# Kernel tuning notes

Measured on AMD Instinct MI355X. Metric: run time of the kernel, lower is better.

## Reference

```python
import jax, jax.numpy as jnp
import numpy as np

HEAD_NUM = 16
SCALE = 1.0 / np.sqrt(HEAD_NUM)  # source divides by sqrt(head_num), not head_dim
MASK_VAL = -10000000.0


def setup_inputs() -> dict:
    key = jax.random.key(0)
    kq, kk, kv = jax.random.split(key, 3)
    shape = (2, 16, 2048, 64)  # [B, H, L, D]
    Q = jax.random.normal(kq, shape, dtype=jnp.float32)
    K = jax.random.normal(kk, shape, dtype=jnp.float32)
    V = jax.random.normal(kv, shape, dtype=jnp.float32)
    return {"Q": Q, "K": K, "V": V}


def reference(Q, K, V):
    L = Q.shape[-2]
    # [B, H, L, M] attention logits, scaled by 1/sqrt(head_num)
    logits = jnp.einsum('bhld,bhmd->bhlm', Q, K) * SCALE
    # causal mask: strictly-upper triangle gets -1e7 (additive, as in source)
    mask = jnp.triu(jnp.ones((L, L), dtype=logits.dtype), 1) * MASK_VAL
    logits = logits + mask[None, None, :, :]
    weights = jax.nn.softmax(logits, axis=-1)
    return jnp.einsum('bhlm,bhmd->bhld', weights, V)
```

## Files before the change

### kernel.cpp

```cpp
#include <hip/hip_runtime.h>
#include <hip/hip_bf16.h>

#define BM 128
#define BN 64
#define HD 64
#define LQ 2048
#define SD 72

typedef __attribute__((ext_vector_type(8))) short short8;
typedef __attribute__((ext_vector_type(16))) float f32x16;

#define QSCALE 0.360673760222241f

#define WS_HALF  ((size_t)32 * 2048 * 64)
#define WS_NEEDED (2 * WS_HALF * sizeof(unsigned short))

static __device__ __forceinline__ unsigned pk2(float a, float b) {
    union { __hip_bfloat162 h2; unsigned u; } c;
    c.h2 = __float22bfloat162_rn(make_float2(a, b));
    return c.u;
}

__global__ __launch_bounds__(256)
void prep(const float* __restrict__ Kg, const float* __restrict__ Vg,
          unsigned short* __restrict__ KF, unsigned short* __restrict__ VF) {
    __shared__ unsigned short sK2[64][72];
    __shared__ unsigned short sV2[64][72];
    const int t  = threadIdx.x;
    const int bx = blockIdx.x;
    const int bh = bx >> 5;
    const int c  = bx & 31;
    const size_t ibase = (size_t)bh * (LQ * HD) + (size_t)c * 64 * HD;
    const int r  = t >> 4;
    const int c4 = (t & 15) * 4;

#pragma unroll
    for (int p = 0; p < 4; ++p) {
        const int row = p * 16 + r;
        const float4 kv4 = *(const float4*)(Kg + ibase + (size_t)row * HD + c4);
        uint2 ku; ku.x = pk2(kv4.x, kv4.y); ku.y = pk2(kv4.z, kv4.w);
        *(uint2*)&sK2[row][c4] = ku;
        const float4 vv4 = *(const float4*)(Vg + ibase + (size_t)row * HD + c4);
        const unsigned u0 = pk2(vv4.x, vv4.y);
        const unsigned u1 = pk2(vv4.z, vv4.w);
        sV2[c4 + 0][row] = (unsigned short)(u0 & 0xffff);
        sV2[c4 + 1][row] = (unsigned short)(u0 >> 16);
        sV2[c4 + 2][row] = (unsigned short)(u1 & 0xffff);
        sV2[c4 + 3][row] = (unsigned short)(u1 >> 16);
    }
    __syncthreads();

    const int lane = t & 63;
    const int u    = t >> 6;
    const int l31  = lane & 31;
    const int hh   = lane >> 5;
#pragma unroll
    for (int e = 0; e < 2; ++e) {
        const int ch = 2 * c + e;
        const size_t ob = ((size_t)(bh * 64 + ch) * 4 + u) * 512 + lane * 8;
        *(uint4*)&KF[ob] = *(const uint4*)&sK2[e * 32 + l31][u * 16 + hh * 8];
        *(uint4*)&VF[ob] = *(const uint4*)&sV2[(u & 1) * 32 + l31][e * 32 + (u >> 1) * 16 + hh * 8];
    }
}

__global__ __launch_bounds__(512, 4)
void fa_main(const float* __restrict__ Qg,
             const unsigned short* __restrict__ KF,
             const unsigned short* __restrict__ VF,
             float* __restrict__ Og) {
    __shared__ float fx[4 * 64 * 32];
    __shared__ float fla[4 * 32];

    const int t    = threadIdx.x;
    const int w    = t >> 6;
    const int lane = t & 63;
    const int h    = lane >> 5;
    const int l31  = lane & 31;
    const int qg   = w & 3;
    const int kp   = w >> 2;

    const int bx  = blockIdx.x;
    const int idx = (bx >> 5) & 7;
    const int qt  = (bx & 256) ? idx : (15 - idx);
    const int bh  = bx & 31;
    const int q0  = qt * BM;

    const size_t base = (size_t)bh * (LQ * HD);
    const unsigned short* KFh = KF + (size_t)bh * 131072 + lane * 8;
    const unsigned short* VFh = VF + (size_t)bh * 131072 + lane * 8;

    const int j    = 4 * qt + qg;
    const int qrow = j * 32 + l31;

    short8 qreg[4];
    {
        const float* Qrow = Qg + base + (size_t)qrow * HD;
#pragma unroll
        for (int ks = 0; ks < 4; ++ks) {
            const float4 a = *(const float4*)(Qrow + ks * 16 + h * 8);
            const float4 b = *(const float4*)(Qrow + ks * 16 + h * 8 + 4);
            union { unsigned u[4]; short8 s8; } qu;
            qu.u[0] = pk2(a.x * QSCALE, a.y * QSCALE);
            qu.u[1] = pk2(a.z * QSCALE, a.w * QSCALE);
            qu.u[2] = pk2(b.x * QSCALE, b.y * QSCALE);
            qu.u[3] = pk2(b.z * QSCALE, b.w * QSCALE);
            qreg[ks] = qu.s8;
        }
    }

    f32x16 accO[2];
#pragma unroll
    for (int r = 0; r < 16; ++r) { accO[0][r] = 0.f; accO[1][r] = 0.f; }
    float lsum = 0.f;

    auto loadK = [&](short8* ak, int ch) {
        const unsigned short* kpt = KFh + (size_t)ch * 2048;
        ak[0] = *(const short8*)(kpt);
        ak[1] = *(const short8*)(kpt + 512);
        ak[2] = *(const short8*)(kpt + 1024);
        ak[3] = *(const short8*)(kpt + 1536);
    };

    auto computech = [&](const short8* ak, short8* akNext, int ch, bool pre) {
        short8 av[4];
        const unsigned short* vp = VFh + (size_t)ch * 2048;
        av[0] = *(const short8*)(vp);
        av[1] = *(const short8*)(vp + 512);
        av[2] = *(const short8*)(vp + 1024);
        av[3] = *(const short8*)(vp + 1536);
        if (pre) loadK(akNext, ch + 2);
        __builtin_amdgcn_sched_barrier(0);

        f32x16 accS;
#pragma unroll
        for (int r = 0; r < 16; ++r) accS[r] = 0.f;
        __builtin_amdgcn_s_setprio(1);
#pragma unroll
        for (int ks = 0; ks < 4; ++ks)
            accS = __builtin_amdgcn_mfma_f32_32x32x16_bf16(ak[ks], qreg[ks], accS, 0, 0, 0);
        __builtin_amdgcn_s_setprio(0);

        if (ch == j) {
            const int kvb = ch * 32 + 4 * h;
#pragma unroll
            for (int r = 0; r < 16; ++r) {
                const int kv = kvb + (r & 3) + 8 * (r >> 2);
                if (kv > qrow) accS[r] = -1e30f;
            }
        }

#pragma unroll
        for (int r = 0; r < 16; ++r) {
            const float p = __builtin_amdgcn_exp2f(accS[r]);
            accS[r] = p;
            lsum += p;
        }

        short8 pf[2];
#pragma unroll
        for (int s = 0; s < 2; ++s) {
            const int rb = s * 8;
            const unsigned a0 = pk2(accS[rb + 0], accS[rb + 1]);
            const unsigned b0 = pk2(accS[rb + 4], accS[rb + 5]);
            const unsigned a1 = pk2(accS[rb + 2], accS[rb + 3]);
            const unsigned b1 = pk2(accS[rb + 6], accS[rb + 7]);
            const auto r02 = __builtin_amdgcn_permlane32_swap(a0, b0, 0, 0);
            const auto r13 = __builtin_amdgcn_permlane32_swap(a1, b1, 0, 0);
            union { unsigned u[4]; short8 s8; } pu;
            pu.u[0] = r02[0]; pu.u[1] = r13[0]; pu.u[2] = r02[1]; pu.u[3] = r13[1];
            pf[s] = pu.s8;
        }

        __builtin_amdgcn_s_setprio(1);
#pragma unroll
        for (int s = 0; s < 2; ++s)
#pragma unroll
            for (int dg = 0; dg < 2; ++dg)
                accO[dg] = __builtin_amdgcn_mfma_f32_32x32x16_bf16(av[s * 2 + dg], pf[s], accO[dg], 0, 0, 0);
        __builtin_amdgcn_s_setprio(0);
    };

    short8 akA[4], akB[4];
    int ch = kp;
    if (ch <= j) {
        loadK(akA, ch);
        for (;;) {
            computech(akA, akB, ch, ch + 2 <= j);
            ch += 2;
            if (ch > j) break;
            computech(akB, akA, ch, ch + 2 <= j);
            ch += 2;
            if (ch > j) break;
        }
    }

    lsum += __shfl_xor(lsum, 32);
    if (kp == 1) {
#pragma unroll
        for (int dg = 0; dg < 2; ++dg) {
#pragma unroll
            for (int r = 0; r < 16; ++r) {
                const int d = dg * 32 + (r & 3) + 8 * (r >> 2) + 4 * h;
                fx[(qg * 64 + d) * 32 + l31] = accO[dg][r];
            }
        }
        if (h == 0) fla[qg * 32 + l31] = lsum;
    }
    __syncthreads();
    if (kp == 0) {
        const float inv = 1.0f / (lsum + fla[qg * 32 + l31]);
        float* Op = Og + base + (size_t)qrow * HD;
#pragma unroll
        for (int dg = 0; dg < 2; ++dg) {
#pragma unroll
            for (int rq = 0; rq < 4; ++rq) {
                const int d = dg * 32 + 8 * rq + 4 * h;
                const float* fr = &fx[(qg * 64 + d) * 32 + l31];
                float4 o;
                o.x = (accO[dg][rq * 4 + 0] + fr[0])  * inv;
                o.y = (accO[dg][rq * 4 + 1] + fr[32]) * inv;
                o.z = (accO[dg][rq * 4 + 2] + fr[64]) * inv;
                o.w = (accO[dg][rq * 4 + 3] + fr[96]) * inv;
                *(float4*)(Op + d) = o;
            }
        }
    }
}

__global__ __launch_bounds__(512, 4)
void fa_fwd(const float* __restrict__ Qg,
            const float* __restrict__ Kg,
            const float* __restrict__ Vg,
            float* __restrict__ Og) {
    __shared__ __align__(16) unsigned short lds[(2 * BN + 2 * HD) * SD];
    typedef unsigned short KT[BN][SD];
    typedef unsigned short VT[HD][SD];
    KT* sK  = (KT*)lds;
    VT* sVt = (VT*)(lds + 2 * BN * SD);

    const int t    = threadIdx.x;
    const int w    = t >> 6;
    const int lane = t & 63;
    const int h    = lane >> 5;
    const int l31  = lane & 31;
    const int qd   = lane >> 4;
    const int qg   = w & 3;
    const int kh   = w >> 2;

    const int bx  = blockIdx.x;
    const int idx = (bx >> 5) & 7;
    const int qt  = (bx & 256) ? idx : (15 - idx);
    const int bh  = bx & 31;
    const int q0  = qt * BM;

    const size_t base = (size_t)bh * (LQ * HD);
    const float* Qp = Qg + base + (size_t)q0 * HD;
    const float* Kp = Kg + base;
    const float* Vp = Vg + base;

    const int r0 = t >> 4;
    const int c4 = (t & 15) * 4;
    const int RA = w * 4;

    {
        unsigned short (*sQ)[SD] = (unsigned short (*)[SD])lds;
#pragma unroll
        for (int p = 0; p < 4; ++p) {
            const int r = p * 32 + r0;
            const float4 v = *(const float4*)(Qp + (size_t)r * HD + c4);
            uint2 u;
            u.x = pk2(v.x * QSCALE, v.y * QSCALE);
            u.y = pk2(v.z * QSCALE, v.w * QSCALE);
            *(uint2*)&sQ[r][c4] = u;
        }
    }
    __syncthreads();
    short8 qreg[4];
    {
        unsigned short (*sQ)[SD] = (unsigned short (*)[SD])lds;
#pragma unroll
        for (int ks = 0; ks < 4; ++ks)
            qreg[ks] = *(const short8*)&sQ[qg * 32 + l31][ks * 16 + h * 8];
    }
    __syncthreads();

    float4 kA, kB, vA, vB;
    auto issue = [&](int kv0) {
        kA = *(const float4*)(Kp + (size_t)(kv0 + r0) * HD + c4);
        kB = *(const float4*)(Kp + (size_t)(kv0 + 32 + r0) * HD + c4);
        vA = *(const float4*)(Vp + (size_t)(kv0 + RA + qd) * HD + c4);
        vB = *(const float4*)(Vp + (size_t)(kv0 + 32 + RA + qd) * HD + c4);
    };
    auto vstore = [&](float4 vf, int R, int buf) {
        float e0 = vf.x, e1 = vf.y, e2 = vf.z, e3 = vf.w;
        float s0 = (qd & 2) ? e0 : e2;
        float s1 = (qd & 2) ? e1 : e3;
        s0 = __shfl_xor(s0, 32); s1 = __shfl_xor(s1, 32);
        if (qd & 2) { e0 = s0; e1 = s1; } else { e2 = s0; e3 = s1; }
        s0 = (qd & 1) ? e0 : e1;
        s1 = (qd & 1) ? e2 : e3;
        s0 = __shfl_xor(s0, 16); s1 = __shfl_xor(s1, 16);
        if (qd & 1) { e0 = s0; e2 = s1; } else { e1 = s0; e3 = s1; }
        const int d   = c4 + qd;
        const int col = ((((R >> 3) ^ (d >> 3)) & 7) << 3) | (R & 7);
        uint2 u; u.x = pk2(e0, e1); u.y = pk2(e2, e3);
        *(uint2*)&sVt[buf][d][col] = u;
    };
    auto commit = [&](int buf) {
        { uint2 u; u.x = pk2(kA.x, kA.y); u.y = pk2(kA.z, kA.w);
          *(uint2*)&sK[buf][r0][c4] = u; }
        { uint2 u; u.x = pk2(kB.x, kB.y); u.y = pk2(kB.z, kB.w);
          *(uint2*)&sK[buf][32 + r0][c4] = u; }
        vstore(vA, RA, buf);
        vstore(vB, 32 + RA, buf);
    };

    f32x16 accO[2];
#pragma unroll
    for (int r = 0; r < 16; ++r) { accO[0][r] = 0.f; accO[1][r] = 0.f; }
    float lsum = 0.f;

    const int qminw = q0 + qg * 32;
    const int qmaxw = qminw + 31;
    const int n_it  = (q0 + BM) / BN;

    issue(0);
    commit(0);

    for (int it = 0; it < n_it; ++it) {
        const int kv0 = it * BN;
        const int buf = it & 1;
        __syncthreads();
        const bool more = (it + 1 < n_it);
        if (more) issue(kv0 + BN);

        if (kv0 + kh * 32 <= qmaxw) {
            f32x16 accS;
#pragma unroll
            for (int r = 0; r < 16; ++r) accS[r] = 0.f;
            __builtin_amdgcn_s_setprio(1);
#pragma unroll
            for (int ks = 0; ks < 4; ++ks) {
                const short8 ak = *(const short8*)&sK[buf][kh * 32 + l31][ks * 16 + h * 8];
                accS = __builtin_amdgcn_mfma_f32_32x32x16_bf16(ak, qreg[ks], accS, 0, 0, 0);
            }
            __builtin_amdgcn_s_setprio(0);

            if (kv0 + kh * 32 + 31 > qminw) {
                const int qrow = qminw + l31;
                const int kvb  = kv0 + kh * 32 + 4 * h;
#pragma unroll
                for (int r = 0; r < 16; ++r) {
                    const int kv = kvb + (r & 3) + 8 * (r >> 2);
                    if (kv > qrow) accS[r] = -1e30f;
                }
            }
#pragma unroll
            for (int r = 0; r < 16; ++r) {
                const float p = __builtin_amdgcn_exp2f(accS[r]);
                accS[r] = p;
                lsum += p;
            }
            short8 pf[2];
#pragma unroll
            for (int s = 0; s < 2; ++s) {
                const int rb = s * 8;
                const unsigned a0 = pk2(accS[rb + 0], accS[rb + 1]);
                const unsigned b0 = pk2(accS[rb + 4], accS[rb + 5]);
                const unsigned a1 = pk2(accS[rb + 2], accS[rb + 3]);
                const unsigned b1 = pk2(accS[rb + 6], accS[rb + 7]);
                const auto r02 = __builtin_amdgcn_permlane32_swap(a0, b0, 0, 0);
                const auto r13 = __builtin_amdgcn_permlane32_swap(a1, b1, 0, 0);
                union { unsigned u[4]; short8 s8; } pu;
                pu.u[0] = r02[0]; pu.u[1] = r13[0]; pu.u[2] = r02[1]; pu.u[3] = r13[1];
                pf[s] = pu.s8;
            }
            __builtin_amdgcn_s_setprio(1);
#pragma unroll
            for (int s = 0; s < 2; ++s) {
                const int K0 = kh * 32 + s * 16 + h * 8;
#pragma unroll
                for (int dg = 0; dg < 2; ++dg) {
                    const int d   = dg * 32 + l31;
                    const int col = (((K0 >> 3) ^ (d >> 3)) & 7) << 3;
                    const short8 av = *(const short8*)&sVt[buf][d][col];
                    accO[dg] = __builtin_amdgcn_mfma_f32_32x32x16_bf16(av, pf[s], accO[dg], 0, 0, 0);
                }
            }
            __builtin_amdgcn_s_setprio(0);
        }

        if (more) commit(buf ^ 1);
    }

    lsum += __shfl_xor(lsum, 32);
    __syncthreads();
    float* fx  = (float*)lds;
    float* fla = fx + 4 * 64 * 32;
    if (kh == 1) {
#pragma unroll
        for (int dg = 0; dg < 2; ++dg) {
#pragma unroll
            for (int r = 0; r < 16; ++r) {
                const int d = dg * 32 + (r & 3) + 8 * (r >> 2) + 4 * h;
                fx[(qg * 64 + d) * 32 + l31] = accO[dg][r];
            }
        }
        if (h == 0) fla[qg * 32 + l31] = lsum;
    }
    __syncthreads();
    if (kh == 0) {
        const float inv  = 1.0f / (lsum + fla[qg * 32 + l31]);
        const int   qrow = q0 + qg * 32 + l31;
        float* Op = Og + base + (size_t)qrow * HD;
#pragma unroll
        for (int dg = 0; dg < 2; ++dg) {
#pragma unroll
            for (int rq = 0; rq < 4; ++rq) {
                const int d = dg * 32 + 8 * rq + 4 * h;
                const float* fr = &fx[(qg * 64 + d) * 32 + l31];
                float4 o;
                o.x = (accO[dg][rq * 4 + 0] + fr[0])  * inv;
                o.y = (accO[dg][rq * 4 + 1] + fr[32]) * inv;
                o.z = (accO[dg][rq * 4 + 2] + fr[64]) * inv;
                o.w = (accO[dg][rq * 4 + 3] + fr[96]) * inv;
                *(float4*)(Op + d) = o;
            }
        }
    }
}

extern "C" void kernel_launch(void* const* d_in, const int* in_sizes, int n_in,
                              void* d_out, int out_size, void* d_ws, size_t ws_size,
                              hipStream_t stream) {
    const float* Q = (const float*)d_in[0];
    const float* K = (const float*)d_in[1];
    const float* V = (const float*)d_in[2];
    float* O = (float*)d_out;
    if (d_ws != nullptr && ws_size >= WS_NEEDED) {
        unsigned short* KF = (unsigned short*)d_ws;
        unsigned short* VF = KF + WS_HALF;
        prep<<<dim3(1024), dim3(256), 0, stream>>>(K, V, KF, VF);
        fa_main<<<dim3(512), dim3(512), 0, stream>>>(Q, KF, VF, O);
    } else {
        fa_fwd<<<dim3(512), dim3(512), 0, stream>>>(Q, K, V, O);
    }
}
```

Before: 119.0 us.

## Software-pipeline QK^T of next chunk with softmax and PV of current chunk

```diff
diff --git a/kernel.cpp b/kernel.cpp
--- a/kernel.cpp
+++ b/kernel.cpp
@@ -83,7 +83,6 @@
     const int idx = (bx >> 5) & 7;
     const int qt  = (bx & 256) ? idx : (15 - idx);
     const int bh  = bx & 31;
-    const int q0  = qt * BM;
 
     const size_t base = (size_t)bh * (LQ * HD);
     const unsigned short* KFh = KF + (size_t)bh * 131072 + lane * 8;
@@ -113,25 +112,24 @@
     for (int r = 0; r < 16; ++r) { accO[0][r] = 0.f; accO[1][r] = 0.f; }
     float lsum = 0.f;
 
-    auto loadK = [&](short8* ak, int ch) {
-        const unsigned short* kpt = KFh + (size_t)ch * 2048;
-        ak[0] = *(const short8*)(kpt);
-        ak[1] = *(const short8*)(kpt + 512);
-        ak[2] = *(const short8*)(kpt + 1024);
-        ak[3] = *(const short8*)(kpt + 1536);
-    };
-
-    auto computech = [&](const short8* ak, short8* akNext, int ch, bool pre) {
-        short8 av[4];
-        const unsigned short* vp = VFh + (size_t)ch * 2048;
-        av[0] = *(const short8*)(vp);
-        av[1] = *(const short8*)(vp + 512);
-        av[2] = *(const short8*)(vp + 1024);
-        av[3] = *(const short8*)(vp + 1536);
-        if (pre) loadK(akNext, ch + 2);
-        __builtin_amdgcn_sched_barrier(0);
-
-        f32x16 accS;
+    short8 ak[4], av[4], pf[2];
+    f32x16 accS;
+
+    auto loadK = [&](int ch) {
+        const unsigned short* p = KFh + (size_t)ch * 2048;
+        ak[0] = *(const short8*)(p);
+        ak[1] = *(const short8*)(p + 512);
+        ak[2] = *(const short8*)(p + 1024);
+        ak[3] = *(const short8*)(p + 1536);
+    };
+    auto loadV = [&](int ch) {
+        const unsigned short* p = VFh + (size_t)ch * 2048;
+        av[0] = *(const short8*)(p);
+        av[1] = *(const short8*)(p + 512);
+        av[2] = *(const short8*)(p + 1024);
+        av[3] = *(const short8*)(p + 1536);
+    };
+    auto qkt = [&]() {
 #pragma unroll
         for (int r = 0; r < 16; ++r) accS[r] = 0.f;
         __builtin_amdgcn_s_setprio(1);
@@ -139,24 +137,22 @@
         for (int ks = 0; ks < 4; ++ks)
             accS = __builtin_amdgcn_mfma_f32_32x32x16_bf16(ak[ks], qreg[ks], accS, 0, 0, 0);
         __builtin_amdgcn_s_setprio(0);
-
-        if (ch == j) {
-            const int kvb = ch * 32 + 4 * h;
+    };
+    auto smpk = [&](int pc) {
+        if (pc == j) {
+            const int kvb = pc * 32 + 4 * h;
 #pragma unroll
             for (int r = 0; r < 16; ++r) {
                 const int kv = kvb + (r & 3) + 8 * (r >> 2);
                 if (kv > qrow) accS[r] = -1e30f;
             }
         }
-
 #pragma unroll
         for (int r = 0; r < 16; ++r) {
             const float p = __builtin_amdgcn_exp2f(accS[r]);
             accS[r] = p;
             lsum += p;
         }
-
-        short8 pf[2];
 #pragma unroll
         for (int s = 0; s < 2; ++s) {
             const int rb = s * 8;
@@ -170,7 +166,8 @@
             pu.u[0] = r02[0]; pu.u[1] = r13[0]; pu.u[2] = r02[1]; pu.u[3] = r13[1];
             pf[s] = pu.s8;
         }
-
+    };
+    auto pv = [&]() {
         __builtin_amdgcn_s_setprio(1);
 #pragma unroll
         for (int s = 0; s < 2; ++s)
@@ -180,18 +177,26 @@
         __builtin_amdgcn_s_setprio(0);
     };
 
-    short8 akA[4], akB[4];
     int ch = kp;
     if (ch <= j) {
-        loadK(akA, ch);
-        for (;;) {
-            computech(akA, akB, ch, ch + 2 <= j);
+        loadK(ch);
+        loadV(ch);
+        qkt();
+        int pc = ch;
+        ch += 2;
+        while (ch <= j) {
+            loadK(ch);
+            __builtin_amdgcn_sched_barrier(0);
+            smpk(pc);
+            pv();
+            loadV(ch);
+            __builtin_amdgcn_sched_barrier(0);
+            qkt();
+            pc = ch;
             ch += 2;
-            if (ch > j) break;
-            computech(akB, akA, ch, ch + 2 <= j);
-            ch += 2;
-            if (ch > j) break;
-        }
+        }
+        smpk(pc);
+        pv();
     }
 
     lsum += __shfl_xor(lsum, 32);
```

New measurement: 117.6 us. No clear change (-1.2%).
